# Kernel tuning notes

Measured on AMD Instinct MI355X. Metric: run time of the kernel, lower is better.

Reference implementation:

```python
import jax, jax.numpy as jnp
import numpy as np

B, S, D, H = 2, 2048, 2048, 16
HD = D // H
FF = 4 * D
EPS = 1e-5
SCALE = 1.0 / np.sqrt(D)  # source uses 1/sqrt(d_out), not 1/sqrt(head_dim)


def _gelu_tanh(x):
    c = np.sqrt(2.0 / np.pi).astype(np.float32)
    return 0.5 * x * (1.0 + jnp.tanh(c * (x + 0.044715 * x * x * x)))


def _layernorm(x, scale, shift):
    mean = jnp.mean(x, axis=-1, keepdims=True)
    var = jnp.mean(jnp.square(x - mean), axis=-1, keepdims=True)  # correction=0
    return (x - mean) * jax.lax.rsqrt(var + EPS) * scale + shift


def setup_inputs() -> dict:
    key = jax.random.key(0)
    ks = jax.random.split(key, 10)
    init = lambda k, shape, fan_in: (jax.random.normal(k, shape, jnp.float32) / np.sqrt(fan_in))
    return {
        "x": jax.random.normal(ks[0], (B, S, D), jnp.float32),
        "wq": init(ks[1], (D, D), D),
        "wk": init(ks[2], (D, D), D),
        "wv": init(ks[3], (D, D), D),
        "wo": init(ks[4], (D, D), D),
        "bo": jnp.zeros((D,), jnp.float32),
        "g1": jnp.ones((D,), jnp.float32),
        "s1": jnp.zeros((D,), jnp.float32),
        "g2": jnp.ones((D,), jnp.float32),
        "s2": jnp.zeros((D,), jnp.float32),
        "w1": init(ks[5], (D, FF), D),
        "b1": jnp.zeros((FF,), jnp.float32),
        "w2": init(ks[6], (FF, D), FF),
        "b2": jnp.zeros((D,), jnp.float32),
    }


def _block(x, wq, wk, wv, wo, bo, g1, s1, g2, s2, w1, b1, w2, b2):
    # pre-LN attention
    h = _layernorm(x, g1, s1)
    q = (h @ wq).reshape(B, S, H, HD).transpose(0, 2, 1, 3)  # [B,H,S,HD]
    k = (h @ wk).reshape(B, S, H, HD).transpose(0, 2, 1, 3)
    v = (h @ wv).reshape(B, S, H, HD).transpose(0, 2, 1, 3)
    scores = jnp.einsum('bhqd,bhkd->bhqk', q, k) * SCALE
    causal = jnp.tril(jnp.ones((S, S), dtype=bool))  # mask strictly-upper
    scores = jnp.where(causal, scores, -jnp.inf)
    attn = jax.nn.softmax(scores, axis=-1)
    ctx = jnp.einsum('bhqk,bhkd->bhqd', attn, v)
    ctx = ctx.transpose(0, 2, 1, 3).reshape(B, S, D)
    x = x + ctx @ wo + bo
    # pre-LN FFN
    h = _layernorm(x, g2, s2)
    h = _gelu_tanh(h @ w1 + b1) @ w2 + b2
    return x + h


def reference(x, wq, wk, wv, wo, bo, g1, s1, g2, s2, w1, b1, w2, b2):
    return _block(x, wq, wk, wv, wo, bo, g1, s1, g2, s2, w1, b1, w2, b2)
```

## Files before the change

kernel.cpp:

```cpp
#include <hip/hip_runtime.h>
#include <hip/hip_bf16.h>
#include <cstdint>

constexpr float SCALE_QK = 0.02209708691207961f;

using short8 = __attribute__((ext_vector_type(8))) short;
using f32x4  = __attribute__((ext_vector_type(4))) float;
using ushort4v = __attribute__((ext_vector_type(4))) ushort;

#define MFMA16(a,b,c) __builtin_amdgcn_mfma_f32_16x16x32_bf16((a),(b),(c),0,0,0)

__device__ __forceinline__ ushort f2bf(float f){
  uint32_t u = __builtin_bit_cast(uint32_t, f);
  u += 0x7fffu + ((u >> 16) & 1u);
  return (ushort)(u >> 16);
}

__device__ __forceinline__ void gload_lds16(const void* g, void* l){
  __builtin_amdgcn_global_load_lds(
      (const __attribute__((address_space(1))) void*)g,
      (__attribute__((address_space(3))) void*)l, 16, 0, 0);
}

__global__ __launch_bounds__(256) void ln_kernel(
    const float* __restrict__ x, const float* __restrict__ g,
    const float* __restrict__ sh, ushort* __restrict__ out){
  const int row = blockIdx.x, t = threadIdx.x;
  const float* xr = x + (size_t)row*2048 + t*8;
  float v[8];
  *(float4*)&v[0] = *(const float4*)(xr);
  *(float4*)&v[4] = *(const float4*)(xr + 4);
  float s = 0.f, sq = 0.f;
#pragma unroll
  for (int i = 0; i < 8; ++i){ s += v[i]; sq += v[i]*v[i]; }
#pragma unroll
  for (int d = 1; d < 64; d <<= 1){ s += __shfl_xor(s, d, 64); sq += __shfl_xor(sq, d, 64); }
  __shared__ float red[8];
  const int w = t >> 6, lane = t & 63;
  if (lane == 0){ red[w] = s; red[4 + w] = sq; }
  __syncthreads();
  s  = red[0] + red[1] + red[2] + red[3];
  sq = red[4] + red[5] + red[6] + red[7];
  const float mean = s * (1.f/2048.f);
  const float inv  = rsqrtf(sq * (1.f/2048.f) - mean*mean + 1e-5f);
  union { ushort u[8]; uint4 v4; } o;
#pragma unroll
  for (int i = 0; i < 8; ++i){
    int j = t*8 + i;
    o.u[i] = f2bf((v[i] - mean) * inv * g[j] + sh[j]);
  }
  *(uint4*)(out + (size_t)row*2048 + t*8) = o.v4;
}

__global__ __launch_bounds__(256) void wconv_t(
    const float* __restrict__ in, ushort* __restrict__ out, int K, int N){
  __shared__ ushort tile[32][34];
  const int tx = threadIdx.x & 31, ty = threadIdx.x >> 5;
  const int n0 = blockIdx.x * 32, k0 = blockIdx.y * 32;
#pragma unroll
  for (int r = 0; r < 4; ++r){
    int kk = ty + r*8;
    tile[kk][tx] = f2bf(in[(size_t)(k0 + kk)*N + n0 + tx]);
  }
  __syncthreads();
#pragma unroll
  for (int r = 0; r < 4; ++r){
    int nn = ty + r*8;
    out[(size_t)(n0 + nn)*K + k0 + tx] = tile[tx][nn];
  }
}

template<int EPI>
__global__ __launch_bounds__(256) void gemm_bt(
    const ushort* __restrict__ A, const ushort* __restrict__ Bt,
    int N, int K, void* __restrict__ outp,
    const float* __restrict__ resid, const float* __restrict__ bias){
  __shared__ ushort lds[2][128*64];
  const int tid = threadIdx.x, lane = tid & 63, wid = tid >> 6;
  const int wr = wid >> 1, wc = wid & 1;
  const int l15 = lane & 15, l4 = lane >> 4;

  const int bid = blockIdx.x;
  const int xcd = bid & 7, j = bid >> 3;
  const int mb = xcd*4 + (j & 3);
  const int nb = j >> 2;
  const int m0 = mb * 128, n0 = nb * 128;

  f32x4 acc[4][4];
#pragma unroll
  for (int mi = 0; mi < 4; ++mi)
#pragma unroll
    for (int ni = 0; ni < 4; ++ni) acc[mi][ni] = (f32x4){0.f,0.f,0.f,0.f};

  const ushort* Abase = A  + (size_t)m0*K;
  const ushort* Bbase = Bt + (size_t)n0*K;

  const int NTk = K >> 6;
  for (int kt = 0; kt < NTk; ++kt){
    if (kt) __syncthreads();
#pragma unroll
    for (int i = 0; i < 4; ++i){
      const int chunk = (i*4 + wid)*64 + lane;
      const int row = chunk >> 3;
      const int c8  = (chunk & 7) ^ (row & 7);
      const size_t goff = (size_t)row*K + (size_t)kt*64 + c8*8;
      gload_lds16(Abase + goff, (ushort*)&lds[0][0] + (size_t)(i*4 + wid)*512);
      gload_lds16(Bbase + goff, (ushort*)&lds[1][0] + (size_t)(i*4 + wid)*512);
    }
    __syncthreads();

#pragma unroll
    for (int kk = 0; kk < 2; ++kk){
      short8 af[4], bf[4];
      const int kb = kk*4 + l4;
#pragma unroll
      for (int i = 0; i < 4; ++i){
        const int rA = wr*64 + i*16 + l15;
        af[i] = *(const short8*)&lds[0][rA*64 + ((kb ^ (rA & 7))*8)];
        const int rB = wc*64 + i*16 + l15;
        bf[i] = *(const short8*)&lds[1][rB*64 + ((kb ^ (rB & 7))*8)];
      }
#pragma unroll
      for (int mi = 0; mi < 4; ++mi)
#pragma unroll
        for (int ni = 0; ni < 4; ++ni)
          acc[mi][ni] = MFMA16(af[mi], bf[ni], acc[mi][ni]);
    }
  }

  if constexpr (EPI == 0){
    __syncthreads();
    ushort* tile = (ushort*)&lds[0][0];
    const int which = n0 >> 11;
    const int hh = (n0 & 2047) >> 7;
    const int bb = m0 >> 11, srow0 = m0 & 2047;
    if (which != 2){
      const float qs = (which == 0) ? SCALE_QK : 1.0f;
#pragma unroll
      for (int mi = 0; mi < 4; ++mi)
#pragma unroll
        for (int ni = 0; ni < 4; ++ni){
          const int rl = wr*64 + mi*16 + l4*4;
          const int cl = wc*64 + ni*16 + l15;
#pragma unroll
          for (int j2 = 0; j2 < 4; ++j2)
            tile[(rl + j2)*128 + cl] = f2bf(acc[mi][ni][j2] * qs);
        }
      __syncthreads();
      ushort* dst = (ushort*)outp + (size_t)which*8388608 +
                    ((size_t)(bb*16 + hh)*2048 + srow0)*128;
#pragma unroll
      for (int i = 0; i < 8; ++i){
        const int c = i*256 + tid, row = c >> 4, d8 = (c & 15)*8;
        *(uint4*)(dst + (size_t)row*128 + d8) = *(const uint4*)&tile[row*128 + d8];
      }
    } else {
#pragma unroll
      for (int mi = 0; mi < 4; ++mi)
#pragma unroll
        for (int ni = 0; ni < 4; ++ni){
          const int rl = wr*64 + mi*16 + l4*4;
          const int cl = wc*64 + ni*16 + l15;
          ushort4v o;
#pragma unroll
          for (int j2 = 0; j2 < 4; ++j2) o[j2] = f2bf(acc[mi][ni][j2]);
          *(ushort4v*)&tile[cl*128 + rl] = o;
        }
      __syncthreads();
      ushort* dst = (ushort*)outp + (size_t)2*8388608 +
                    (size_t)(bb*16 + hh)*262144 + srow0;
#pragma unroll
      for (int i = 0; i < 8; ++i){
        const int c = i*256 + tid, drow = c >> 4, s8 = (c & 15)*8;
        *(uint4*)(dst + (size_t)drow*2048 + s8) = *(const uint4*)&tile[drow*128 + s8];
      }
    }
  } else {
#pragma unroll
    for (int mi = 0; mi < 4; ++mi){
#pragma unroll
      for (int ni = 0; ni < 4; ++ni){
        const int rloc = wr*64 + mi*16 + l4*4;
        const int col  = n0 + wc*64 + ni*16 + l15;
#pragma unroll
        for (int j2 = 0; j2 < 4; ++j2){
          const int m = m0 + rloc + j2;
          float v = acc[mi][ni][j2];
          if constexpr (EPI == 1){
            ((float*)outp)[(size_t)m*N + col] = resid[(size_t)m*N + col] + bias[col] + v;
          } else {
            const float xx = v + bias[col];
            const float z  = 0.7978845608f*(xx + 0.044715f*xx*xx*xx);
            const float t  = __expf(-2.f*fabsf(z));
            const float th = (1.f - t)/(1.f + t);
            const float gl = 0.5f*xx*(1.f + copysignf(th, xx));
            ((ushort*)outp)[(size_t)m*N + col] = f2bf(gl);
          }
        }
      }
    }
  }
}

__global__ __launch_bounds__(256, 2) void attn_kernel(
    const ushort* __restrict__ q, const ushort* __restrict__ k,
    const ushort* __restrict__ vt, ushort* __restrict__ ctx){
  __shared__ ushort k_lds[2][64*128];
  __shared__ ushort v_lds[2][128*64];
  __shared__ ushort p_lds[4][32*64];
  const int tid = threadIdx.x, lane = tid & 63, w = tid >> 6;
  const int l15 = lane & 15, l4 = lane >> 4;
  const int id = blockIdx.x;
  const int bh = id & 31;
  const int r  = id >> 5;
  const int qt = (r < 8) ? (15 - r) : (r - 8);
  const int bb = bh >> 4, hh = bh & 15;
  const ushort* kbase = k  + (size_t)bh * 262144;
  const ushort* vbase = vt + (size_t)bh * 262144;

  short8 qf[2][4];
#pragma unroll
  for (int mi = 0; mi < 2; ++mi){
    const int s = qt*128 + w*32 + mi*16 + l15;
    const ushort* qr = q + ((size_t)bh*2048 + s)*128 + l4*8;
#pragma unroll
    for (int kk = 0; kk < 4; ++kk) qf[mi][kk] = *(const short8*)(qr + kk*32);
  }

  f32x4 cacc[2][8];
#pragma unroll
  for (int mi = 0; mi < 2; ++mi)
#pragma unroll
    for (int dt = 0; dt < 8; ++dt) cacc[mi][dt] = (f32x4){0.f,0.f,0.f,0.f};
  float mrun[2][4], lrun[2][4];
#pragma unroll
  for (int mi = 0; mi < 2; ++mi)
#pragma unroll
    for (int j = 0; j < 4; ++j){ mrun[mi][j] = -1e30f; lrun[mi][j] = 0.f; }

  auto stage = [&](int buf, int t){
    const ushort* ksrc = kbase + (size_t)t*8192;
#pragma unroll
    for (int i = 0; i < 4; ++i){
      const int base = i*256 + w*64;
      const int chunk = base + lane;
      const int kr = chunk >> 4;
      const int c8 = (chunk & 15) ^ (kr & 7);
      gload_lds16(ksrc + (size_t)kr*128 + c8*8, &k_lds[buf][(size_t)base*8]);
    }
#pragma unroll
    for (int i = 0; i < 4; ++i){
      const int base = i*256 + w*64;
      const int chunk = base + lane;
      const int vr = chunk >> 3;
      const int c8 = (chunk & 7) ^ (vr & 7);
      gload_lds16(vbase + (size_t)vr*2048 + t*64 + c8*8, &v_lds[buf][(size_t)base*8]);
    }
  };

  const int nt = 2*qt + 2;
  stage(0, 0);
  __syncthreads();
  int cur = 0;
  for (int t = 0; t < nt; ++t){
    if (t + 1 < nt) stage(cur ^ 1, t + 1);

    const bool skip = (t == 2*qt + 1) && (w < 2);
    if (!skip){
      f32x4 sa[2][4];
#pragma unroll
      for (int mi = 0; mi < 2; ++mi)
#pragma unroll
        for (int ct = 0; ct < 4; ++ct) sa[mi][ct] = (f32x4){0.f,0.f,0.f,0.f};
      __builtin_amdgcn_s_setprio(1);
#pragma unroll
      for (int kk = 0; kk < 4; ++kk){
#pragma unroll
        for (int ct = 0; ct < 4; ++ct){
          const int kr = ct*16 + l15;
          short8 kf = *(const short8*)&k_lds[cur][kr*128 + (((kk*4 + l4) ^ (kr & 7))*8)];
          sa[0][ct] = MFMA16(qf[0][kk], kf, sa[0][ct]);
          sa[1][ct] = MFMA16(qf[1][kk], kf, sa[1][ct]);
        }
      }
      __builtin_amdgcn_s_setprio(0);

      const bool anymask = (t >= 2*qt) && !((t == 2*qt) && (w >= 2));
#pragma unroll
      for (int mi = 0; mi < 2; ++mi){
#pragma unroll
        for (int j = 0; j < 4; ++j){
          const int qa = qt*128 + w*32 + mi*16 + l4*4 + j;
          float mnew = mrun[mi][j];
#pragma unroll
          for (int ct = 0; ct < 4; ++ct){
            float sc = sa[mi][ct][j];
            if (anymask){
              const int ka = t*64 + ct*16 + l15;
              sc = (ka > qa) ? -1e30f : sc;
            }
            sa[mi][ct][j] = sc;
            mnew = fmaxf(mnew, sc);
          }
#pragma unroll
          for (int d = 1; d < 16; d <<= 1) mnew = fmaxf(mnew, __shfl_xor(mnew, d, 16));
          const float corr = __expf(mrun[mi][j] - mnew);
          mrun[mi][j] = mnew; lrun[mi][j] *= corr;
          float psum = 0.f;
#pragma unroll
          for (int ct = 0; ct < 4; ++ct){
            const float p = __expf(sa[mi][ct][j] - mnew);
            sa[mi][ct][j] = p; psum += p;
          }
          lrun[mi][j] += psum;
#pragma unroll
          for (int dt = 0; dt < 8; ++dt) cacc[mi][dt][j] *= corr;
        }
      }

#pragma unroll
      for (int mi = 0; mi < 2; ++mi)
#pragma unroll
        for (int ct = 0; ct < 4; ++ct)
#pragma unroll
          for (int j = 0; j < 4; ++j){
            const int row = mi*16 + l4*4 + j, col = ct*16 + l15;
            p_lds[w][row*64 + ((col >> 3) ^ (row & 7))*8 + (col & 7)] = f2bf(sa[mi][ct][j]);
          }

      __builtin_amdgcn_s_setprio(1);
#pragma unroll
      for (int kk2 = 0; kk2 < 2; ++kk2){
        const int kb = kk2*4 + l4;
        short8 pa0 = *(const short8*)&p_lds[w][l15*64 + ((kb ^ (l15 & 7))*8)];
        short8 pa1 = *(const short8*)&p_lds[w][(16 + l15)*64 + ((kb ^ (l15 & 7))*8)];
#pragma unroll
        for (int dt = 0; dt < 8; ++dt){
          const int vr = dt*16 + l15;
          short8 vf = *(const short8*)&v_lds[cur][vr*64 + ((kb ^ (vr & 7))*8)];
          cacc[0][dt] = MFMA16(pa0, vf, cacc[0][dt]);
          cacc[1][dt] = MFMA16(pa1, vf, cacc[1][dt]);
        }
      }
      __builtin_amdgcn_s_setprio(0);
    }

    if (t + 1 < nt){ __syncthreads(); cur ^= 1; }
  }

#pragma unroll
  for (int mi = 0; mi < 2; ++mi){
    float inv[4];
#pragma unroll
    for (int j = 0; j < 4; ++j){
      float lt = lrun[mi][j];
#pragma unroll
      for (int d = 1; d < 16; d <<= 1) lt += __shfl_xor(lt, d, 16);
      inv[j] = 1.f / lt;
    }
#pragma unroll
    for (int dt = 0; dt < 8; ++dt)
#pragma unroll
      for (int j = 0; j < 4; ++j){
        const int s = qt*128 + w*32 + mi*16 + l4*4 + j;
        const int d = dt*16 + l15;
        ctx[((size_t)(bb*2048 + s))*2048 + hh*128 + d] = f2bf(cacc[mi][dt][j] * inv[j]);
      }
  }
}

extern "C" void kernel_launch(void* const* d_in, const int* in_sizes, int n_in,
                              void* d_out, int out_size, void* d_ws, size_t ws_size,
                              hipStream_t stream) {
  const float* x  = (const float*)d_in[0];
  const float* wq = (const float*)d_in[1];
  const float* wk = (const float*)d_in[2];
  const float* wv = (const float*)d_in[3];
  const float* wo = (const float*)d_in[4];
  const float* bo = (const float*)d_in[5];
  const float* g1 = (const float*)d_in[6];
  const float* s1 = (const float*)d_in[7];
  const float* g2 = (const float*)d_in[8];
  const float* s2 = (const float*)d_in[9];
  const float* w1 = (const float*)d_in[10];
  const float* b1 = (const float*)d_in[11];
  const float* w2 = (const float*)d_in[12];
  const float* b2 = (const float*)d_in[13];
  float* out = (float*)d_out;
  char* ws = (char*)d_ws;

  ushort* wqkvT = (ushort*)(ws + 0);
  ushort* wkT = (ushort*)(ws + 8388608);
  ushort* wvT = (ushort*)(ws + 16777216);
  ushort* woT = (ushort*)(ws + 25165824);
  ushort* w1T = (ushort*)(ws + 33554432);
  ushort* w2T = (ushort*)(ws + 67108864);
  ushort* h1  = (ushort*)(ws + 100663296);
  ushort* qb  = (ushort*)(ws + 117440512);
  ushort* kb  = (ushort*)(ws + 134217728);
  ushort* vtb = (ushort*)(ws + 150994944);
  ushort* ctxb= (ushort*)(ws + 184549376);
  float*  x2  = (float*)(ws + 201326592);
  ushort* h2  = (ushort*)(ws + 234881024);
  ushort* ffb = (ushort*)(ws + 117440512);

  wconv_t<<<dim3(64, 64), 256, 0, stream>>>(wq, wqkvT, 2048, 2048);
  wconv_t<<<dim3(64, 64), 256, 0, stream>>>(wk, wkT, 2048, 2048);
  wconv_t<<<dim3(64, 64), 256, 0, stream>>>(wv, wvT, 2048, 2048);
  wconv_t<<<dim3(64, 64), 256, 0, stream>>>(wo, woT, 2048, 2048);
  wconv_t<<<dim3(256, 64), 256, 0, stream>>>(w1, w1T, 2048, 8192);
  wconv_t<<<dim3(64, 256), 256, 0, stream>>>(w2, w2T, 8192, 2048);

  ln_kernel<<<4096, 256, 0, stream>>>(x, g1, s1, h1);

  gemm_bt<0><<<32*48, 256, 0, stream>>>(h1, wqkvT, 6144, 2048, qb, nullptr, nullptr);

  attn_kernel<<<512, 256, 0, stream>>>(qb, kb, vtb, ctxb);

  gemm_bt<1><<<32*16, 256, 0, stream>>>(ctxb, woT, 2048, 2048, x2, x, bo);

  ln_kernel<<<4096, 256, 0, stream>>>(x2, g2, s2, h2);

  gemm_bt<2><<<32*64, 256, 0, stream>>>(h2, w1T, 8192, 2048, ffb, nullptr, b1);
  gemm_bt<1><<<32*16, 256, 0, stream>>>(ffb, w2T, 2048, 8192, out, x2, b2);

  (void)in_sizes; (void)n_in; (void)out_size; (void)ws_size;
}
```

Before: 688.7 us.

## Use exp2 softmax with lazy max rescaling and merge square weight conversions

Folds log2(e) into the Q scaling so the attention softmax can use exp2f in place of __expf. The running max and the rescaling of the accumulator are now updated only when some row's tile max exceeds the stored max by more than 8, and that check is taken wave-wide with __any. This skips the cross-lane shuffles and the corr multiplies on most tiles. The four 2048x2048 weight transposes are also merged into one launch. The lazy rescale allows unnormalized values up to 2^8, which bf16 P and fp32 accumulators must absorb.

```diff
diff --git a/kernel.cpp b/kernel.cpp
--- a/kernel.cpp
+++ b/kernel.cpp
@@ -3,6 +3,7 @@
 #include <cstdint>
 
 constexpr float SCALE_QK = 0.02209708691207961f;
+constexpr float LOG2E    = 1.4426950408889634f;
 
 using short8 = __attribute__((ext_vector_type(8))) short;
 using f32x4  = __attribute__((ext_vector_type(4))) float;
@@ -70,6 +71,28 @@
   }
 }
 
+__global__ __launch_bounds__(256) void wconv4(
+    const float* __restrict__ w0, const float* __restrict__ w1p,
+    const float* __restrict__ w2p, const float* __restrict__ w3p,
+    ushort* __restrict__ out){
+  __shared__ ushort tile[32][34];
+  const int tx = threadIdx.x & 31, ty = threadIdx.x >> 5;
+  const int n0 = blockIdx.x * 32, k0 = blockIdx.y * 32, z = blockIdx.z;
+  const float* in = (z == 0) ? w0 : (z == 1) ? w1p : (z == 2) ? w2p : w3p;
+  ushort* o = out + (size_t)z * 4194304;
+#pragma unroll
+  for (int r = 0; r < 4; ++r){
+    int kk = ty + r*8;
+    tile[kk][tx] = f2bf(in[(size_t)(k0 + kk)*2048 + n0 + tx]);
+  }
+  __syncthreads();
+#pragma unroll
+  for (int r = 0; r < 4; ++r){
+    int nn = ty + r*8;
+    o[(size_t)(n0 + nn)*2048 + k0 + tx] = tile[tx][nn];
+  }
+}
+
 template<int EPI>
 __global__ __launch_bounds__(256) void gemm_bt(
     const ushort* __restrict__ A, const ushort* __restrict__ Bt,
@@ -135,7 +158,7 @@
     const int hh = (n0 & 2047) >> 7;
     const int bb = m0 >> 11, srow0 = m0 & 2047;
     if (which != 2){
-      const float qs = (which == 0) ? SCALE_QK : 1.0f;
+      const float qs = (which == 0) ? SCALE_QK * LOG2E : 1.0f;
 #pragma unroll
       for (int mi = 0; mi < 4; ++mi)
 #pragma unroll
@@ -286,12 +309,14 @@
       __builtin_amdgcn_s_setprio(0);
 
       const bool anymask = (t >= 2*qt) && !((t == 2*qt) && (w >= 2));
+      float rowlm[2][4];
+      bool over = false;
 #pragma unroll
       for (int mi = 0; mi < 2; ++mi){
 #pragma unroll
         for (int j = 0; j < 4; ++j){
           const int qa = qt*128 + w*32 + mi*16 + l4*4 + j;
-          float mnew = mrun[mi][j];
+          float lm = -1e30f;
 #pragma unroll
           for (int ct = 0; ct < 4; ++ct){
             float sc = sa[mi][ct][j];
@@ -300,23 +325,39 @@
               sc = (ka > qa) ? -1e30f : sc;
             }
             sa[mi][ct][j] = sc;
-            mnew = fmaxf(mnew, sc);
+            lm = fmaxf(lm, sc);
           }
-#pragma unroll
-          for (int d = 1; d < 16; d <<= 1) mnew = fmaxf(mnew, __shfl_xor(mnew, d, 16));
-          const float corr = __expf(mrun[mi][j] - mnew);
-          mrun[mi][j] = mnew; lrun[mi][j] *= corr;
+          rowlm[mi][j] = lm;
+          over = over || (lm > mrun[mi][j] + 8.f);
+        }
+      }
+      if (__any(over)){
+#pragma unroll
+        for (int mi = 0; mi < 2; ++mi)
+#pragma unroll
+          for (int j = 0; j < 4; ++j){
+            float mx = rowlm[mi][j];
+#pragma unroll
+            for (int d = 1; d < 16; d <<= 1) mx = fmaxf(mx, __shfl_xor(mx, d, 16));
+            const float mnew = fmaxf(mrun[mi][j], mx);
+            const float corr = exp2f(mrun[mi][j] - mnew);
+            mrun[mi][j] = mnew; lrun[mi][j] *= corr;
+#pragma unroll
+            for (int dt = 0; dt < 8; ++dt) cacc[mi][dt][j] *= corr;
+          }
+      }
+#pragma unroll
+      for (int mi = 0; mi < 2; ++mi)
+#pragma unroll
+        for (int j = 0; j < 4; ++j){
           float psum = 0.f;
 #pragma unroll
           for (int ct = 0; ct < 4; ++ct){
-            const float p = __expf(sa[mi][ct][j] - mnew);
+            const float p = exp2f(sa[mi][ct][j] - mrun[mi][j]);
             sa[mi][ct][j] = p; psum += p;
           }
           lrun[mi][j] += psum;
-#pragma unroll
-          for (int dt = 0; dt < 8; ++dt) cacc[mi][dt][j] *= corr;
-        }
-      }
+        }
 
 #pragma unroll
       for (int mi = 0; mi < 2; ++mi)
@@ -390,8 +431,6 @@
   char* ws = (char*)d_ws;
 
   ushort* wqkvT = (ushort*)(ws + 0);
-  ushort* wkT = (ushort*)(ws + 8388608);
-  ushort* wvT = (ushort*)(ws + 16777216);
   ushort* woT = (ushort*)(ws + 25165824);
   ushort* w1T = (ushort*)(ws + 33554432);
   ushort* w2T = (ushort*)(ws + 67108864);
@@ -404,10 +443,7 @@
   ushort* h2  = (ushort*)(ws + 234881024);
   ushort* ffb = (ushort*)(ws + 117440512);
 
-  wconv_t<<<dim3(64, 64), 256, 0, stream>>>(wq, wqkvT, 2048, 2048);
-  wconv_t<<<dim3(64, 64), 256, 0, stream>>>(wk, wkT, 2048, 2048);
-  wconv_t<<<dim3(64, 64), 256, 0, stream>>>(wv, wvT, 2048, 2048);
-  wconv_t<<<dim3(64, 64), 256, 0, stream>>>(wo, woT, 2048, 2048);
+  wconv4<<<dim3(64, 64, 4), 256, 0, stream>>>(wq, wk, wv, wo, wqkvT);
   wconv_t<<<dim3(256, 64), 256, 0, stream>>>(w1, w1T, 2048, 8192);
   wconv_t<<<dim3(64, 256), 256, 0, stream>>>(w2, w2T, 8192, 2048);
 
```

Measured after the change: 673.0 us. -2.3%, faster.
